# Performance work log

Hardware: AMD Instinct MI355X
Metric: run time of the kernel (lower is better)

The kernel has to match this reference:

```python
import jax, jax.numpy as jnp
import numpy as np

VOCAB = 100000
EMBED = 128
N_INNER = VOCAB - 1
MAX_PATH = 20
BATCH = 32768


def setup_inputs() -> dict:
    key = jax.random.key(0)
    k1, k2, k3, k4, k5, k6, k7 = jax.random.split(key, 7)
    center = jax.random.randint(k1, (BATCH,), 0, VOCAB)
    target = jax.random.randint(k2, (BATCH,), 0, VOCAB)
    # embedding table (module inits uniform(-0.5/d, 0.5/d)); inner vectors init zero,
    # but we use small random values so gradients/scores are non-trivial.
    init_range = 0.5 / EMBED
    in_emb = jax.random.uniform(k3, (VOCAB, EMBED), jnp.float32, -init_range, init_range)
    inner_vec = jax.random.normal(k4, (N_INNER, EMBED), jnp.float32) * 0.01
    # Huffman buffers: per-word path lengths between 8 and MAX_PATH, padded with 0.
    lengths = jax.random.randint(k5, (VOCAB, 1), 8, MAX_PATH + 1)          # (V,1)
    pos = jnp.arange(MAX_PATH)[None, :]                                     # (1,L)
    masks = (pos < lengths).astype(jnp.float32)                             # (V,L)
    paths = jax.random.randint(k6, (VOCAB, MAX_PATH), 0, N_INNER) * (pos < lengths)
    # codes are +/-1 on valid positions (word2vec sign labels), 0 on padding
    codes = (2.0 * jax.random.randint(k7, (VOCAB, MAX_PATH), 0, 2).astype(jnp.float32) - 1.0) * masks
    return {"center": center, "target": target, "in_emb": in_emb,
            "inner_vec": inner_vec, "paths": paths, "codes": codes, "masks": masks}


def reference(center, target, in_emb, inner_vec, paths, codes, masks):
    h = in_emb[center]                      # (B, D) center word vectors
    p = paths[target]                       # (B, L) inner-node ids along Huffman path
    c = codes[target]                       # (B, L) +/-1 direction labels
    m = masks[target]                       # (B, L) valid-position mask
    iv = inner_vec[p]                       # (B, L, D) gathered inner-node vectors
    scores = jnp.einsum('bld,bd->bl', iv, h)            # batched matvec
    log_probs = jax.nn.log_sigmoid(c * scores)          # (B, L)
    loss = -(log_probs * m).sum(axis=1)                 # masked path sum
    return loss.mean()
```

## Files before the change

kernel.cpp:

```cpp
#include <hip/hip_runtime.h>

#define VOCAB 100000
#define EMBED 128
#define MAX_PATH 20
#define BATCH 32768
#define WPB 4

__global__ __launch_bounds__(256) void hs_loss_kernel(
    const int* __restrict__ center, const int* __restrict__ target,
    const float* __restrict__ in_emb, const float* __restrict__ inner_vec,
    const int* __restrict__ paths, const float* __restrict__ codes,
    float* __restrict__ partials)
{
    const int wave = threadIdx.x >> 6;
    const int lane = threadIdx.x & 63;
    const int g    = lane >> 4;
    const int gl   = lane & 15;
    const int b = blockIdx.x * WPB + wave;

    const int c = center[b];
    const int t = target[b];

    const float4* hp = (const float4*)(in_emb + (size_t)c * EMBED);
    const float4 h0 = hp[2 * gl];
    const float4 h1 = hp[2 * gl + 1];

    const int   base = t * MAX_PATH + g;
    int   p[5];
    float cd[5];
    #pragma unroll
    for (int j = 0; j < 5; ++j) {
        p[j]  = paths[base + 4 * j];
        cd[j] = codes[base + 4 * j];
    }

    float acc = 0.f;
    #pragma unroll
    for (int j = 0; j < 5; ++j) {
        if (j >= 2) {
            if (__ballot(cd[j] != 0.f) == 0ull) break;
        }
        const float4* ivp = (const float4*)(inner_vec + (size_t)p[j] * EMBED);
        const float4 a0 = ivp[2 * gl];
        const float4 a1 = ivp[2 * gl + 1];
        float d = h0.x * a0.x;
        d = fmaf(h0.y, a0.y, d);
        d = fmaf(h0.z, a0.z, d);
        d = fmaf(h0.w, a0.w, d);
        d = fmaf(h1.x, a1.x, d);
        d = fmaf(h1.y, a1.y, d);
        d = fmaf(h1.z, a1.z, d);
        d = fmaf(h1.w, a1.w, d);
        d += __shfl_xor(d, 1, 64);
        d += __shfl_xor(d, 2, 64);
        d += __shfl_xor(d, 4, 64);
        d += __shfl_xor(d, 8, 64);
        const float x  = cd[j] * d;
        const float ls = fminf(x, 0.f) - __logf(1.f + __expf(-fabsf(x)));
        acc = fmaf(fabsf(cd[j]), ls, acc);
    }

    acc += __shfl_xor(acc, 16, 64);
    acc += __shfl_xor(acc, 32, 64);

    __shared__ float ws[WPB];
    if (lane == 0) ws[wave] = -acc;
    __syncthreads();
    if (threadIdx.x == 0) {
        float s = 0.f;
        #pragma unroll
        for (int i = 0; i < WPB; ++i) s += ws[i];
        partials[blockIdx.x] = s;
    }
}

__global__ __launch_bounds__(256) void hs_reduce_kernel(
    const float* __restrict__ partials, int n, float* __restrict__ out)
{
    float s = 0.f;
    for (int i = threadIdx.x; i < n; i += 256) s += partials[i];
    #pragma unroll
    for (int off = 32; off; off >>= 1) s += __shfl_xor(s, off, 64);
    __shared__ float ws[4];
    const int wave = threadIdx.x >> 6;
    const int lane = threadIdx.x & 63;
    if (lane == 0) ws[wave] = s;
    __syncthreads();
    if (threadIdx.x == 0) {
        out[0] = (ws[0] + ws[1] + ws[2] + ws[3]) / (float)BATCH;
    }
}

extern "C" void kernel_launch(void* const* d_in, const int* in_sizes, int n_in,
                              void* d_out, int out_size, void* d_ws, size_t ws_size,
                              hipStream_t stream) {
    const int*   center    = (const int*)d_in[0];
    const int*   target    = (const int*)d_in[1];
    const float* in_emb    = (const float*)d_in[2];
    const float* inner_vec = (const float*)d_in[3];
    const int*   paths     = (const int*)d_in[4];
    const float* codes     = (const float*)d_in[5];
    float* out = (float*)d_out;
    float* partials = (float*)d_ws;

    const int nblocks = BATCH / WPB;
    hs_loss_kernel<<<nblocks, 256, 0, stream>>>(
        center, target, in_emb, inner_vec, paths, codes, partials);
    hs_reduce_kernel<<<1, 256, 0, stream>>>(partials, nblocks, out);
}
```

Measured before the change: 166.3 us.

## Prefetch all path vectors up front and fuse final reduction via atomic counter

Issues all five inner-vector gathers per lane before computing, removing the ballot-based early exit so the loads can be in flight together. Replaces the separate reduction kernel with a last-block-done pattern using an atomic counter and thread fences, with a memset to reset the counter. This trades extra loads of padded rows for more overlapped memory latency and one fewer kernel launch, though the memset adds its own launch.

```diff
diff --git a/kernel.cpp b/kernel.cpp
--- a/kernel.cpp
+++ b/kernel.cpp
@@ -5,12 +5,14 @@
 #define MAX_PATH 20
 #define BATCH 32768
 #define WPB 4
+#define NBLOCKS (BATCH / WPB)
 
 __global__ __launch_bounds__(256) void hs_loss_kernel(
     const int* __restrict__ center, const int* __restrict__ target,
     const float* __restrict__ in_emb, const float* __restrict__ inner_vec,
     const int* __restrict__ paths, const float* __restrict__ codes,
-    float* __restrict__ partials)
+    float* __restrict__ partials, unsigned int* __restrict__ counter,
+    float* __restrict__ out)
 {
     const int wave = threadIdx.x >> 6;
     const int lane = threadIdx.x & 63;
@@ -25,7 +27,7 @@
     const float4 h0 = hp[2 * gl];
     const float4 h1 = hp[2 * gl + 1];
 
-    const int   base = t * MAX_PATH + g;
+    const int base = t * MAX_PATH + g;
     int   p[5];
     float cd[5];
     #pragma unroll
@@ -34,23 +36,25 @@
         cd[j] = codes[base + 4 * j];
     }
 
+    float4 a0[5], a1[5];
+    #pragma unroll
+    for (int j = 0; j < 5; ++j) {
+        const float4* ivp = (const float4*)(inner_vec + (size_t)p[j] * EMBED);
+        a0[j] = ivp[2 * gl];
+        a1[j] = ivp[2 * gl + 1];
+    }
+
     float acc = 0.f;
     #pragma unroll
     for (int j = 0; j < 5; ++j) {
-        if (j >= 2) {
-            if (__ballot(cd[j] != 0.f) == 0ull) break;
-        }
-        const float4* ivp = (const float4*)(inner_vec + (size_t)p[j] * EMBED);
-        const float4 a0 = ivp[2 * gl];
-        const float4 a1 = ivp[2 * gl + 1];
-        float d = h0.x * a0.x;
-        d = fmaf(h0.y, a0.y, d);
-        d = fmaf(h0.z, a0.z, d);
-        d = fmaf(h0.w, a0.w, d);
-        d = fmaf(h1.x, a1.x, d);
-        d = fmaf(h1.y, a1.y, d);
-        d = fmaf(h1.z, a1.z, d);
-        d = fmaf(h1.w, a1.w, d);
+        float d = h0.x * a0[j].x;
+        d = fmaf(h0.y, a0[j].y, d);
+        d = fmaf(h0.z, a0[j].z, d);
+        d = fmaf(h0.w, a0[j].w, d);
+        d = fmaf(h1.x, a1[j].x, d);
+        d = fmaf(h1.y, a1[j].y, d);
+        d = fmaf(h1.z, a1[j].z, d);
+        d = fmaf(h1.w, a1[j].w, d);
         d += __shfl_xor(d, 1, 64);
         d += __shfl_xor(d, 2, 64);
         d += __shfl_xor(d, 4, 64);
@@ -59,35 +63,31 @@
         const float ls = fminf(x, 0.f) - __logf(1.f + __expf(-fabsf(x)));
         acc = fmaf(fabsf(cd[j]), ls, acc);
     }
-
     acc += __shfl_xor(acc, 16, 64);
     acc += __shfl_xor(acc, 32, 64);
 
     __shared__ float ws[WPB];
+    __shared__ bool  last;
     if (lane == 0) ws[wave] = -acc;
     __syncthreads();
     if (threadIdx.x == 0) {
+        partials[blockIdx.x] = ws[0] + ws[1] + ws[2] + ws[3];
+        __threadfence();
+        unsigned int old = atomicAdd(counter, 1u);
+        last = (old == NBLOCKS - 1);
+    }
+    __syncthreads();
+    if (last) {
+        __threadfence();
         float s = 0.f;
+        for (int i = threadIdx.x; i < NBLOCKS; i += 256) s += partials[i];
         #pragma unroll
-        for (int i = 0; i < WPB; ++i) s += ws[i];
-        partials[blockIdx.x] = s;
-    }
-}
-
-__global__ __launch_bounds__(256) void hs_reduce_kernel(
-    const float* __restrict__ partials, int n, float* __restrict__ out)
-{
-    float s = 0.f;
-    for (int i = threadIdx.x; i < n; i += 256) s += partials[i];
-    #pragma unroll
-    for (int off = 32; off; off >>= 1) s += __shfl_xor(s, off, 64);
-    __shared__ float ws[4];
-    const int wave = threadIdx.x >> 6;
-    const int lane = threadIdx.x & 63;
-    if (lane == 0) ws[wave] = s;
-    __syncthreads();
-    if (threadIdx.x == 0) {
-        out[0] = (ws[0] + ws[1] + ws[2] + ws[3]) / (float)BATCH;
+        for (int off = 32; off; off >>= 1) s += __shfl_xor(s, off, 64);
+        __shared__ float fin[WPB];
+        if ((threadIdx.x & 63) == 0) fin[threadIdx.x >> 6] = s;
+        __syncthreads();
+        if (threadIdx.x == 0)
+            out[0] = (fin[0] + fin[1] + fin[2] + fin[3]) / (float)BATCH;
     }
 }
 
@@ -101,10 +101,12 @@
     const int*   paths     = (const int*)d_in[4];
     const float* codes     = (const float*)d_in[5];
     float* out = (float*)d_out;
-    float* partials = (float*)d_ws;
 
-    const int nblocks = BATCH / WPB;
-    hs_loss_kernel<<<nblocks, 256, 0, stream>>>(
-        center, target, in_emb, inner_vec, paths, codes, partials);
-    hs_reduce_kernel<<<1, 256, 0, stream>>>(partials, nblocks, out);
+    unsigned int* counter  = (unsigned int*)d_ws;
+    float*        partials = (float*)((char*)d_ws + 256);
+
+    hipMemsetAsync(d_ws, 0, 256, stream);
+    hs_loss_kernel<<<NBLOCKS, 256, 0, stream>>>(
+        center, target, in_emb, inner_vec, paths, codes,
+        partials, counter, out);
 }
```

Measured after the change: 483.9 us. 2.91x slower.

## Split each row across 8 lanes to process 8 path nodes per pass

Applied to the files above, without the earlier changes.

Each batch row's dot products are now split across 8 lanes instead of 16, so a wave handles 8 path positions at once and covers the 20 positions in three unrolled passes. The early-exit ballot on padded positions is removed. The first two inner vectors are loaded up front and the third is issued before the second is consumed, to keep more loads in flight. This cuts shuffle steps and loop overhead. In exchange each lane holds more registers, and padded positions now fetch row 0 of the inner-vector table instead of being skipped.

```diff
diff --git a/kernel.cpp b/kernel.cpp
--- a/kernel.cpp
+++ b/kernel.cpp
@@ -5,6 +5,7 @@
 #define MAX_PATH 20
 #define BATCH 32768
 #define WPB 4
+#define NBLOCKS (BATCH / WPB)
 
 __global__ __launch_bounds__(256) void hs_loss_kernel(
     const int* __restrict__ center, const int* __restrict__ target,
@@ -14,52 +15,86 @@
 {
     const int wave = threadIdx.x >> 6;
     const int lane = threadIdx.x & 63;
-    const int g    = lane >> 4;
-    const int gl   = lane & 15;
+    const int g    = lane >> 3;
+    const int gl   = lane & 7;
     const int b = blockIdx.x * WPB + wave;
 
     const int c = center[b];
     const int t = target[b];
 
-    const float4* hp = (const float4*)(in_emb + (size_t)c * EMBED);
-    const float4 h0 = hp[2 * gl];
-    const float4 h1 = hp[2 * gl + 1];
+    const float4* hp = (const float4*)(in_emb + (size_t)c * EMBED) + 4 * gl;
+    const float4 h0 = hp[0], h1 = hp[1], h2 = hp[2], h3 = hp[3];
 
-    const int   base = t * MAX_PATH + g;
-    int   p[5];
-    float cd[5];
-    #pragma unroll
-    for (int j = 0; j < 5; ++j) {
-        p[j]  = paths[base + 4 * j];
-        cd[j] = codes[base + 4 * j];
-    }
+    const int base = t * MAX_PATH + g;
+    const int  p0 = paths[base];
+    const int  p1 = paths[base + 8];
+    const int  off2 = (g < 4) ? 16 : 0;
+    const int  p2 = paths[base + off2];
+    const float c0 = codes[base];
+    const float c1 = codes[base + 8];
+    const float c2 = (g < 4) ? codes[base + 16] : 0.f;
+
+    const float4* v0 = (const float4*)(inner_vec + (size_t)p0 * EMBED) + 4 * gl;
+    float4 a0 = v0[0], a1 = v0[1], a2 = v0[2], a3 = v0[3];
+    const float4* v1 = (const float4*)(inner_vec + (size_t)p1 * EMBED) + 4 * gl;
+    float4 b0 = v1[0], b1 = v1[1], b2 = v1[2], b3 = v1[3];
 
     float acc = 0.f;
-    #pragma unroll
-    for (int j = 0; j < 5; ++j) {
-        if (j >= 2) {
-            if (__ballot(cd[j] != 0.f) == 0ull) break;
-        }
-        const float4* ivp = (const float4*)(inner_vec + (size_t)p[j] * EMBED);
-        const float4 a0 = ivp[2 * gl];
-        const float4 a1 = ivp[2 * gl + 1];
-        float d = h0.x * a0.x;
-        d = fmaf(h0.y, a0.y, d);
-        d = fmaf(h0.z, a0.z, d);
-        d = fmaf(h0.w, a0.w, d);
-        d = fmaf(h1.x, a1.x, d);
-        d = fmaf(h1.y, a1.y, d);
-        d = fmaf(h1.z, a1.z, d);
-        d = fmaf(h1.w, a1.w, d);
+    {
+        float d  = h0.x * a0.x;  d = fmaf(h0.y, a0.y, d);
+        d = fmaf(h0.z, a0.z, d); d = fmaf(h0.w, a0.w, d);
+        float e  = h1.x * a1.x;  e = fmaf(h1.y, a1.y, e);
+        e = fmaf(h1.z, a1.z, e); e = fmaf(h1.w, a1.w, e);
+        d = fmaf(h2.x, a2.x, d); d = fmaf(h2.y, a2.y, d);
+        d = fmaf(h2.z, a2.z, d); d = fmaf(h2.w, a2.w, d);
+        e = fmaf(h3.x, a3.x, e); e = fmaf(h3.y, a3.y, e);
+        e = fmaf(h3.z, a3.z, e); e = fmaf(h3.w, a3.w, e);
+        d += e;
         d += __shfl_xor(d, 1, 64);
         d += __shfl_xor(d, 2, 64);
         d += __shfl_xor(d, 4, 64);
-        d += __shfl_xor(d, 8, 64);
-        const float x  = cd[j] * d;
+        const float x  = c0 * d;
         const float ls = fminf(x, 0.f) - __logf(1.f + __expf(-fabsf(x)));
-        acc = fmaf(fabsf(cd[j]), ls, acc);
+        acc = fmaf(fabsf(c0), ls, acc);
+    }
+    const float4* v2 = (const float4*)(inner_vec + (size_t)p2 * EMBED) + 4 * gl;
+    float4 q0 = v2[0], q1 = v2[1], q2 = v2[2], q3 = v2[3];
+    {
+        float d  = h0.x * b0.x;  d = fmaf(h0.y, b0.y, d);
+        d = fmaf(h0.z, b0.z, d); d = fmaf(h0.w, b0.w, d);
+        float e  = h1.x * b1.x;  e = fmaf(h1.y, b1.y, e);
+        e = fmaf(h1.z, b1.z, e); e = fmaf(h1.w, b1.w, e);
+        d = fmaf(h2.x, b2.x, d); d = fmaf(h2.y, b2.y, d);
+        d = fmaf(h2.z, b2.z, d); d = fmaf(h2.w, b2.w, d);
+        e = fmaf(h3.x, b3.x, e); e = fmaf(h3.y, b3.y, e);
+        e = fmaf(h3.z, b3.z, e); e = fmaf(h3.w, b3.w, e);
+        d += e;
+        d += __shfl_xor(d, 1, 64);
+        d += __shfl_xor(d, 2, 64);
+        d += __shfl_xor(d, 4, 64);
+        const float x  = c1 * d;
+        const float ls = fminf(x, 0.f) - __logf(1.f + __expf(-fabsf(x)));
+        acc = fmaf(fabsf(c1), ls, acc);
+    }
+    {
+        float d  = h0.x * q0.x;  d = fmaf(h0.y, q0.y, d);
+        d = fmaf(h0.z, q0.z, d); d = fmaf(h0.w, q0.w, d);
+        float e  = h1.x * q1.x;  e = fmaf(h1.y, q1.y, e);
+        e = fmaf(h1.z, q1.z, e); e = fmaf(h1.w, q1.w, e);
+        d = fmaf(h2.x, q2.x, d); d = fmaf(h2.y, q2.y, d);
+        d = fmaf(h2.z, q2.z, d); d = fmaf(h2.w, q2.w, d);
+        e = fmaf(h3.x, q3.x, e); e = fmaf(h3.y, q3.y, e);
+        e = fmaf(h3.z, q3.z, e); e = fmaf(h3.w, q3.w, e);
+        d += e;
+        d += __shfl_xor(d, 1, 64);
+        d += __shfl_xor(d, 2, 64);
+        d += __shfl_xor(d, 4, 64);
+        const float x  = c2 * d;
+        const float ls = fminf(x, 0.f) - __logf(1.f + __expf(-fabsf(x)));
+        acc = fmaf(fabsf(c2), ls, acc);
     }
 
+    acc += __shfl_xor(acc, 8, 64);
     acc += __shfl_xor(acc, 16, 64);
     acc += __shfl_xor(acc, 32, 64);
 
@@ -67,18 +102,15 @@
     if (lane == 0) ws[wave] = -acc;
     __syncthreads();
     if (threadIdx.x == 0) {
-        float s = 0.f;
-        #pragma unroll
-        for (int i = 0; i < WPB; ++i) s += ws[i];
-        partials[blockIdx.x] = s;
+        partials[blockIdx.x] = ws[0] + ws[1] + ws[2] + ws[3];
     }
 }
 
 __global__ __launch_bounds__(256) void hs_reduce_kernel(
-    const float* __restrict__ partials, int n, float* __restrict__ out)
+    const float* __restrict__ partials, float* __restrict__ out)
 {
     float s = 0.f;
-    for (int i = threadIdx.x; i < n; i += 256) s += partials[i];
+    for (int i = threadIdx.x; i < NBLOCKS; i += 256) s += partials[i];
     #pragma unroll
     for (int off = 32; off; off >>= 1) s += __shfl_xor(s, off, 64);
     __shared__ float ws[4];
@@ -103,8 +135,7 @@
     float* out = (float*)d_out;
     float* partials = (float*)d_ws;
 
-    const int nblocks = BATCH / WPB;
-    hs_loss_kernel<<<nblocks, 256, 0, stream>>>(
+    hs_loss_kernel<<<NBLOCKS, 256, 0, stream>>>(
         center, target, in_emb, inner_vec, paths, codes, partials);
-    hs_reduce_kernel<<<1, 256, 0, stream>>>(partials, nblocks, out);
+    hs_reduce_kernel<<<1, 256, 0, stream>>>(partials, out);
 }
```

New measurement: 177.9 us. +7.0%, slower.
